# Kernel optimization log

Hardware: AMD Instinct MI355X
Metric: run time of the kernel (lower is better)

## Reference

```python
import jax, jax.numpy as jnp
import numpy as np

B, N, D = 4, 2048, 1024
H, HD = 16, 64          # heads, head dim
ROT = 64                # rotary dims (full head)
SCALE = HD ** -0.5


def _rotate_half(x):
    # interleaved pair rotation: (c r) with r=2 -> (-x2, x1)
    x = x.reshape(x.shape[:-1] + (-1, 2))
    x1, x2 = x[..., 0], x[..., 1]
    return jnp.stack((-x2, x1), axis=-1).reshape(x.shape[:-2] + (-1,))


def _rope(t, pos_enc):
    # t: [b,h,n,c], pos_enc: [1,n,rot] -> broadcast over heads
    pe = pos_enc[:, None, : t.shape[-2], :]          # [1,1,n,rot]
    t_rot, t_pass = t[..., :ROT], t[..., ROT:]
    t_rot = t_rot * jnp.cos(pe) + _rotate_half(t_rot) * jnp.sin(pe)
    return jnp.concatenate((t_rot, t_pass), axis=-1)


def setup_inputs() -> dict:
    key = jax.random.key(0)
    ks = jax.random.split(key, 16)
    s = 0.02
    return {
        "query": jax.random.normal(ks[0], (B, N, D), jnp.float32),
        "key": jax.random.normal(ks[1], (B, N, D), jnp.float32),
        "value": jax.random.normal(ks[2], (B, N, D), jnp.float32),
        "pad_mask": jax.random.randint(ks[3], (B, N), 0, 2) > 0,
        "pos_enc": jax.random.uniform(ks[4], (1, N, ROT), jnp.float32),
        "Wq": jax.random.normal(ks[5], (D, D), jnp.float32) * s,
        "bq": jnp.zeros((D,), jnp.float32),
        "Wk": jax.random.normal(ks[6], (D, D), jnp.float32) * s,
        "bk": jnp.zeros((D,), jnp.float32),
        "Wv": jax.random.normal(ks[7], (D, D), jnp.float32) * s,
        "bv": jnp.zeros((D,), jnp.float32),
        "Wo": jax.random.normal(ks[8], (D, D), jnp.float32) * s,
        "bo": jnp.zeros((D,), jnp.float32),
    }


def reference(query, key, value, pad_mask, pos_enc, Wq, bq, Wk, bk, Wv, bv, Wo, bo):
    def split_heads(x):
        return x.reshape(x.shape[0], x.shape[1], H, HD).transpose(0, 2, 1, 3)  # b h n c

    q = split_heads(query @ Wq + bq) * SCALE
    k = split_heads(key @ Wk + bk)
    v = split_heads(value @ Wv + bv)

    q = _rope(q, pos_enc)
    k = _rope(k, pos_enc)

    attn = jnp.einsum("bhic,bhjc->bhij", q, k)
    neg = -jnp.finfo(attn.dtype).max
    attn = jnp.where(pad_mask[:, None, None, :], neg, attn)
    attn = jax.nn.softmax(attn, axis=-1)

    o = jnp.einsum("bhij,bhjc->bhic", attn, v)
    o = o.transpose(0, 2, 1, 3).reshape(o.shape[0], o.shape[2], H * HD)  # b n (h c)
    return o @ Wo + bo
```

## Files before the change

kernel.cpp:

```cpp
#include <hip/hip_runtime.h>

#define B_ 4
#define N_ 2048
#define D_ 1024
#define H_ 16
#define HD_ 64
#define QSCALE_ 0.18033688011112042f

typedef __bf16 bf16x8 __attribute__((ext_vector_type(8)));
typedef float f32x4 __attribute__((ext_vector_type(4)));

#if __has_builtin(__builtin_amdgcn_exp2f)
#define EXP2(x) __builtin_amdgcn_exp2f(x)
#else
#define EXP2(x) exp2f(x)
#endif

__device__ __forceinline__ f32x4 mfma16(bf16x8 a, bf16x8 b, f32x4 c) {
    return __builtin_amdgcn_mfma_f32_16x16x32_bf16(a, b, c, 0, 0, 0);
}

__device__ __forceinline__ void gload16(const void* g, void* l) {
    __builtin_amdgcn_global_load_lds(
        (const __attribute__((address_space(1))) void*)g,
        (__attribute__((address_space(3))) void*)l, 16, 0, 0);
}

__device__ __forceinline__ unsigned pack2(float x, float y) {
    __bf16 a = (__bf16)x, b = (__bf16)y;
    unsigned ua = __builtin_bit_cast(unsigned short, a);
    unsigned ub = __builtin_bit_cast(unsigned short, b);
    return ua | (ub << 16);
}

__global__ void prep_kernel(const float* __restrict__ pe, const int* __restrict__ mask,
                            unsigned* __restrict__ cstab, float* __restrict__ maskf) {
    int i = blockIdx.x * 256 + threadIdx.x;
    if (i < N_ * HD_) {
        float v = pe[i];
        __bf16 cb = (__bf16)cosf(v), sb = (__bf16)sinf(v);
        unsigned cu = __builtin_bit_cast(unsigned short, cb);
        unsigned su = __builtin_bit_cast(unsigned short, sb);
        cstab[i] = cu | (su << 16);
    }
    if (i < B_ * N_) maskf[i] = mask[i] ? -1e30f : 0.0f;
}

__global__ __launch_bounds__(256) void tw_kernel(const float* __restrict__ W, __bf16* __restrict__ Wt) {
    __shared__ float T[64][65];
    const int k0 = blockIdx.x * 64, n0 = blockIdx.y * 64;
    const int t = threadIdx.x;
#pragma unroll
    for (int i = 0; i < 4; ++i) {
        int row = i * 16 + (t >> 4);
        int c4 = (t & 15) * 4;
        float4 v = *(const float4*)(W + (size_t)(k0 + row) * D_ + n0 + c4);
        T[row][c4] = v.x; T[row][c4 + 1] = v.y; T[row][c4 + 2] = v.z; T[row][c4 + 3] = v.w;
    }
    __syncthreads();
#pragma unroll
    for (int i = 0; i < 2; ++i) {
        int task = i * 256 + t;
        int nrow = task >> 3, ks = task & 7;
        bf16x8 o;
#pragma unroll
        for (int e = 0; e < 8; ++e) o[e] = (__bf16)T[ks * 8 + e][nrow];
        *(bf16x8*)(Wt + (size_t)(n0 + nrow) * D_ + k0 + ks * 8) = o;
    }
}

__global__ __launch_bounds__(256) void tw3_kernel(
    const float* __restrict__ W0, const float* __restrict__ W1, const float* __restrict__ W2,
    __bf16* __restrict__ T0, __bf16* __restrict__ T1, __bf16* __restrict__ T2)
{
    const float* W = (blockIdx.z == 0) ? W0 : (blockIdx.z == 1) ? W1 : W2;
    __bf16* Wt = (blockIdx.z == 0) ? T0 : (blockIdx.z == 1) ? T1 : T2;
    __shared__ float T[64][65];
    const int k0 = blockIdx.x * 64, n0 = blockIdx.y * 64;
    const int t = threadIdx.x;
#pragma unroll
    for (int i = 0; i < 4; ++i) {
        int row = i * 16 + (t >> 4);
        int c4 = (t & 15) * 4;
        float4 v = *(const float4*)(W + (size_t)(k0 + row) * D_ + n0 + c4);
        T[row][c4] = v.x; T[row][c4 + 1] = v.y; T[row][c4 + 2] = v.z; T[row][c4 + 3] = v.w;
    }
    __syncthreads();
#pragma unroll
    for (int i = 0; i < 2; ++i) {
        int task = i * 256 + t;
        int nrow = task >> 3, ks = task & 7;
        bf16x8 o;
#pragma unroll
        for (int e = 0; e < 8; ++e) o[e] = (__bf16)T[ks * 8 + e][nrow];
        *(bf16x8*)(Wt + (size_t)(n0 + nrow) * D_ + k0 + ks * 8) = o;
    }
}

__global__ __launch_bounds__(256) void proj_v5(
    const float* __restrict__ Xq, const float* __restrict__ Xk, const float* __restrict__ Xv,
    const __bf16* __restrict__ WtQ, const __bf16* __restrict__ WtK, const __bf16* __restrict__ WtV,
    const float* __restrict__ bQ, const float* __restrict__ bK, const float* __restrict__ bV,
    const unsigned* __restrict__ cstab,
    __bf16* __restrict__ dq, __bf16* __restrict__ dk, __bf16* __restrict__ dv)
{
    __shared__ __align__(16) char smem[35072];
    __bf16* As = (__bf16*)smem;
    __bf16* Bs = (__bf16*)(smem + 16384);

    const int which = blockIdx.y >> 3;
    const float* X    = (which == 0) ? Xq  : (which == 1) ? Xk  : Xv;
    const __bf16* Wt  = (which == 0) ? WtQ : (which == 1) ? WtK : WtV;
    const float* bias = (which == 0) ? bQ  : (which == 1) ? bK  : bV;
    __bf16* dst       = (which == 0) ? dq  : (which == 1) ? dk  : dv;
    const int mode = which;

    const int tid = threadIdx.x;
    const int lane = tid & 63, w = tid >> 6;
    const int wr = w >> 1, wc = w & 1;
    const int r16 = lane & 15, g = lane >> 4;
    const int m0 = blockIdx.x * 128;
    const int n0 = (blockIdx.y & 7) * 128;
    const int srow8 = tid >> 3, slot = tid & 7;

    f32x4 acc[4][4];
#pragma unroll
    for (int m = 0; m < 4; ++m)
#pragma unroll
        for (int n = 0; n < 4; ++n) acc[m][n] = (f32x4){0.f, 0.f, 0.f, 0.f};

    for (int kt = 0; kt < 16; ++kt) {
        float4 va0[4], va1[4];
#pragma unroll
        for (int i = 0; i < 4; ++i) {
            int row = i * 32 + srow8;
            const float* s = X + (size_t)(m0 + row) * D_ + kt * 64 + slot * 8;
            va0[i] = *(const float4*)s;
            va1[i] = *(const float4*)(s + 4);
        }
#pragma unroll
        for (int j = 0; j < 4; ++j) {
            int row = j * 32 + srow8;
            const char* src = (const char*)Wt + ((size_t)(n0 + row) * D_ + kt * 64) * 2
                              + ((slot ^ (row & 7)) << 4);
            gload16(src, (char*)Bs + j * 4096 + w * 1024);
        }
#pragma unroll
        for (int i = 0; i < 4; ++i) {
            int row = i * 32 + srow8;
            bf16x8 bv;
            bv[0] = (__bf16)va0[i].x; bv[1] = (__bf16)va0[i].y;
            bv[2] = (__bf16)va0[i].z; bv[3] = (__bf16)va0[i].w;
            bv[4] = (__bf16)va1[i].x; bv[5] = (__bf16)va1[i].y;
            bv[6] = (__bf16)va1[i].z; bv[7] = (__bf16)va1[i].w;
            *(bf16x8*)((char*)As + row * 128 + ((slot ^ (row & 7)) << 4)) = bv;
        }
        __syncthreads();
#pragma unroll
        for (int kk = 0; kk < 2; ++kk) {
            bf16x8 aF[4], bF[4];
#pragma unroll
            for (int m = 0; m < 4; ++m) {
                int row = wr * 64 + m * 16 + r16;
                aF[m] = *(const bf16x8*)((char*)As + row * 128 + (((kk * 4 + g) ^ (row & 7)) << 4));
            }
#pragma unroll
            for (int n = 0; n < 4; ++n) {
                int row = wc * 64 + n * 16 + r16;
                bF[n] = *(const bf16x8*)((char*)Bs + row * 128 + (((kk * 4 + g) ^ (row & 7)) << 4));
            }
#pragma unroll
            for (int m = 0; m < 4; ++m)
#pragma unroll
                for (int n = 0; n < 4; ++n)
                    acc[m][n] = mfma16(aF[m], bF[n], acc[m][n]);
        }
        __syncthreads();
    }

    if (mode <= 1) {
#pragma unroll
        for (int m = 0; m < 4; ++m)
#pragma unroll
            for (int n = 0; n < 4; ++n) {
                int col = n0 + wc * 64 + n * 16 + r16;
                int h = col >> 6, hd = col & 63;
#pragma unroll
                for (int j = 0; j < 4; ++j) {
                    int bn = m0 + wr * 64 + m * 16 + g * 4 + j;
                    int np = bn & (N_ - 1), b = bn >> 11;
                    float val = acc[m][n][j] + bias[col];
                    if (mode == 0) val *= QSCALE_;
                    float other = __shfl_xor(val, 1);
                    unsigned cs = cstab[np * HD_ + hd];
                    float c = __uint_as_float(cs << 16);
                    float sn = __uint_as_float(cs & 0xffff0000u);
                    val = val * c + ((col & 1) ? other : -other) * sn;
                    dst[((size_t)(b * H_ + h) * N_ + np) * HD_ + hd] = (__bf16)val;
                }
            }
    } else {
        __bf16* T = (__bf16*)smem;
#pragma unroll
        for (int m = 0; m < 4; ++m)
#pragma unroll
            for (int n = 0; n < 4; ++n) {
                int c = wc * 64 + n * 16 + r16;
                float bs = bias[n0 + c];
#pragma unroll
                for (int j = 0; j < 4; ++j) {
                    int sr = wr * 64 + m * 16 + g * 4 + j;
                    T[c * 136 + sr] = (__bf16)(acc[m][n][j] + bs);
                }
            }
        __syncthreads();
        const int b = m0 >> 11, np0 = m0 & (N_ - 1);
#pragma unroll
        for (int i = 0; i < 8; ++i) {
            int task = i * 256 + tid;
            int trow = task >> 4, ch = task & 15;
            int colg = n0 + trow;
            int h = colg >> 6, hd = colg & 63;
            bf16x8 vv = *(const bf16x8*)&T[trow * 136 + ch * 8];
            *(bf16x8*)(dst + (((size_t)(b * H_ + h) * HD_ + hd) * N_ + np0 + ch * 8)) = vv;
        }
    }
}

__global__ __launch_bounds__(256, 4) void attn_v6(
    const __bf16* __restrict__ qws, const __bf16* __restrict__ kws,
    const __bf16* __restrict__ vtws, const float* __restrict__ maskf,
    __bf16* __restrict__ ows)
{
    __shared__ __align__(16) __bf16 Ks0[4096], Ks1[4096];
    __shared__ __align__(16) __bf16 Vs0[4096], Vs1[4096];
    __shared__ __align__(16) char Pbuf[8192];

    const int tid = threadIdx.x;
    const int lane = tid & 63, w = tid >> 6;
    const int r16 = lane & 15, g = lane >> 4;

    const int lid = blockIdx.x;
    const int virt = (lid & 7) * 128 + (lid >> 3);
    const int bh = virt >> 4;
    const int b = bh >> 4, h = bh & 15;
    const int q0 = (virt & 15) * 128;
    const int srow8 = tid >> 3, slot = tid & 7;

    bf16x8 qF[2][2];
#pragma unroll
    for (int qq = 0; qq < 2; ++qq) {
        const __bf16* qb = qws + ((size_t)bh * N_ + q0 + w * 32 + qq * 16 + r16) * HD_ + g * 8;
        qF[qq][0] = *(const bf16x8*)qb;
        qF[qq][1] = *(const bf16x8*)(qb + 32);
    }

    bf16x8 onesF;
#pragma unroll
    for (int e = 0; e < 8; ++e) onesF[e] = (__bf16)1.0f;

    const char* kbase = (const char*)(kws + (size_t)bh * N_ * HD_);
    const char* vbase = (const char*)(vtws + (size_t)bh * HD_ * N_);
    const float* mbase = maskf + b * N_;
    char* Pw = Pbuf + w * 2048;

    f32x4 o[2][4];
    f32x4 lacc[2];
#pragma unroll
    for (int qq = 0; qq < 2; ++qq) {
        lacc[qq] = (f32x4){0.f, 0.f, 0.f, 0.f};
#pragma unroll
        for (int n = 0; n < 4; ++n) o[qq][n] = (f32x4){0.f, 0.f, 0.f, 0.f};
    }

#define STAGE_(KD, VD, kt) {                                                          \
    _Pragma("unroll")                                                                 \
    for (int j = 0; j < 2; ++j) {                                                     \
        int row = j * 32 + srow8;                                                     \
        gload16(kbase + (size_t)((kt) * 64 + row) * 128 + ((slot ^ (row & 7)) << 4),  \
                (char*)(KD) + j * 4096 + w * 1024);                                   \
    }                                                                                 \
    _Pragma("unroll")                                                                 \
    for (int j = 0; j < 2; ++j) {                                                     \
        int row = j * 32 + srow8;                                                     \
        gload16(vbase + (size_t)row * (N_ * 2) + (kt) * 128 + ((slot ^ (row & 7)) << 4), \
                (char*)(VD) + j * 4096 + w * 1024);                                   \
    } }

#define TILE_(KB, VB, KN, VN, kt) {                                                   \
    if ((kt) + 1 < 32) STAGE_(KN, VN, (kt) + 1);                                      \
    f32x4 s0[4], s1[4];                                                               \
    _Pragma("unroll")                                                                 \
    for (int n = 0; n < 4; ++n) {                                                     \
        f32x4 mb = *(const f32x4*)(mbase + (kt) * 64 + n * 16 + g * 4);               \
        s0[n] = mb; s1[n] = mb;                                                       \
    }                                                                                 \
    __builtin_amdgcn_s_setprio(1);                                                    \
    _Pragma("unroll")                                                                 \
    for (int n = 0; n < 4; ++n) {                                                     \
        int row = n * 16 + r16;                                                       \
        bf16x8 kF0 = *(const bf16x8*)((const char*)(KB) + row * 128 + ((g ^ (row & 7)) << 4));        \
        bf16x8 kF1 = *(const bf16x8*)((const char*)(KB) + row * 128 + (((4 + g) ^ (row & 7)) << 4));  \
        s0[n] = mfma16(kF0, qF[0][0], s0[n]);                                         \
        s0[n] = mfma16(kF1, qF[0][1], s0[n]);                                         \
        s1[n] = mfma16(kF0, qF[1][0], s1[n]);                                         \
        s1[n] = mfma16(kF1, qF[1][1], s1[n]);                                         \
    }                                                                                 \
    __builtin_amdgcn_s_setprio(0);                                                    \
    bf16x8 pF0[2], pF1[2];                                                            \
    _Pragma("unroll")                                                                 \
    for (int n = 0; n < 4; ++n) {                                                     \
        int u0 = ((n * 2 + (g >> 1)) ^ (r16 & 7));                                    \
        int off = (g & 1) * 2;                                                        \
        *(unsigned*)(Pw + r16 * 128 + u0 * 16 + off * 4)       = pack2(EXP2(s0[n][0]), EXP2(s0[n][1])); \
        *(unsigned*)(Pw + r16 * 128 + u0 * 16 + (off + 1) * 4) = pack2(EXP2(s0[n][2]), EXP2(s0[n][3])); \
    }                                                                                 \
    _Pragma("unroll")                                                                 \
    for (int kk = 0; kk < 2; ++kk)                                                    \
        pF0[kk] = *(const bf16x8*)(Pw + r16 * 128 + (((kk * 4 + g) ^ (r16 & 7)) << 4)); \
    lacc[0] = mfma16(onesF, pF0[0], lacc[0]);                                         \
    lacc[0] = mfma16(onesF, pF0[1], lacc[0]);                                         \
    _Pragma("unroll")                                                                 \
    for (int n = 0; n < 4; ++n) {                                                     \
        int u0 = ((n * 2 + (g >> 1)) ^ (r16 & 7));                                    \
        int off = (g & 1) * 2;                                                        \
        *(unsigned*)(Pw + r16 * 128 + u0 * 16 + off * 4)       = pack2(EXP2(s1[n][0]), EXP2(s1[n][1])); \
        *(unsigned*)(Pw + r16 * 128 + u0 * 16 + (off + 1) * 4) = pack2(EXP2(s1[n][2]), EXP2(s1[n][3])); \
    }                                                                                 \
    _Pragma("unroll")                                                                 \
    for (int kk = 0; kk < 2; ++kk)                                                    \
        pF1[kk] = *(const bf16x8*)(Pw + r16 * 128 + (((kk * 4 + g) ^ (r16 & 7)) << 4)); \
    lacc[1] = mfma16(onesF, pF1[0], lacc[1]);                                         \
    lacc[1] = mfma16(onesF, pF1[1], lacc[1]);                                         \
    __builtin_amdgcn_s_setprio(1);                                                    \
    _Pragma("unroll")                                                                 \
    for (int n = 0; n < 4; ++n) {                                                     \
        int row = n * 16 + r16;                                                       \
        bf16x8 vF0 = *(const bf16x8*)((const char*)(VB) + row * 128 + ((g ^ (row & 7)) << 4));        \
        bf16x8 vF1 = *(const bf16x8*)((const char*)(VB) + row * 128 + (((4 + g) ^ (row & 7)) << 4));  \
        o[0][n] = mfma16(vF0, pF0[0], o[0][n]);                                       \
        o[0][n] = mfma16(vF1, pF0[1], o[0][n]);                                       \
        o[1][n] = mfma16(vF0, pF1[0], o[1][n]);                                       \
        o[1][n] = mfma16(vF1, pF1[1], o[1][n]);                                       \
    }                                                                                 \
    __builtin_amdgcn_s_setprio(0);                                                    \
    __syncthreads(); }

    STAGE_(Ks0, Vs0, 0);
    __syncthreads();

    for (int kt = 0; kt < 32; kt += 2) {
        TILE_(Ks0, Vs0, Ks1, Vs1, kt);
        TILE_(Ks1, Vs1, Ks0, Vs0, kt + 1);
    }
#undef TILE_
#undef STAGE_

#pragma unroll
    for (int qq = 0; qq < 2; ++qq) {
        float inv = 1.0f / lacc[qq][0];
#pragma unroll
        for (int n = 0; n < 4; ++n) {
            int u0 = ((n * 2 + (g >> 1)) ^ (r16 & 7));
            int off = (g & 1) * 2;
            *(unsigned*)(Pw + r16 * 128 + u0 * 16 + off * 4)       = pack2(o[qq][n][0] * inv, o[qq][n][1] * inv);
            *(unsigned*)(Pw + r16 * 128 + u0 * 16 + (off + 1) * 4) = pack2(o[qq][n][2] * inv, o[qq][n][3] * inv);
        }
        int qrow = q0 + w * 32 + qq * 16 + r16;
#pragma unroll
        for (int kk = 0; kk < 2; ++kk) {
            bf16x8 v = *(const bf16x8*)(Pw + r16 * 128 + (((kk * 4 + g) ^ (r16 & 7)) << 4));
            *(bf16x8*)(ows + ((size_t)(b * N_ + qrow)) * D_ + h * HD_ + kk * 32 + g * 8) = v;
        }
    }
}

__global__ __launch_bounds__(256) void gemm_out_v2(
    const __bf16* __restrict__ A, const __bf16* __restrict__ Wt,
    const float* __restrict__ bias, float* __restrict__ out)
{
    __shared__ __align__(16) __bf16 As[8192], Bs[8192];

    const int tid = threadIdx.x;
    const int lane = tid & 63, w = tid >> 6;
    const int wr = w >> 1, wc = w & 1;
    const int r16 = lane & 15, g = lane >> 4;
    const int m0 = blockIdx.x * 128;
    const int n0 = blockIdx.y * 128;
    const int srow8 = tid >> 3, slot = tid & 7;

    f32x4 acc[4][4];
#pragma unroll
    for (int m = 0; m < 4; ++m)
#pragma unroll
        for (int n = 0; n < 4; ++n) acc[m][n] = (f32x4){0.f, 0.f, 0.f, 0.f};

    for (int kt = 0; kt < 16; ++kt) {
#pragma unroll
        for (int j = 0; j < 4; ++j) {
            int row = j * 32 + srow8;
            const char* srcA = (const char*)A + ((size_t)(m0 + row) * D_ + kt * 64) * 2
                               + ((slot ^ (row & 7)) << 4);
            gload16(srcA, (char*)As + j * 4096 + w * 1024);
            const char* srcB = (const char*)Wt + ((size_t)(n0 + row) * D_ + kt * 64) * 2
                               + ((slot ^ (row & 7)) << 4);
            gload16(srcB, (char*)Bs + j * 4096 + w * 1024);
        }
        __syncthreads();
#pragma unroll
        for (int kk = 0; kk < 2; ++kk) {
            bf16x8 aF[4], bF[4];
#pragma unroll
            for (int m = 0; m < 4; ++m) {
                int row = wr * 64 + m * 16 + r16;
                aF[m] = *(const bf16x8*)((char*)As + row * 128 + (((kk * 4 + g) ^ (row & 7)) << 4));
            }
#pragma unroll
            for (int n = 0; n < 4; ++n) {
                int row = wc * 64 + n * 16 + r16;
                bF[n] = *(const bf16x8*)((char*)Bs + row * 128 + (((kk * 4 + g) ^ (row & 7)) << 4));
            }
#pragma unroll
            for (int m = 0; m < 4; ++m)
#pragma unroll
                for (int n = 0; n < 4; ++n)
                    acc[m][n] = mfma16(aF[m], bF[n], acc[m][n]);
        }
        __syncthreads();
    }

#pragma unroll
    for (int m = 0; m < 4; ++m)
#pragma unroll
        for (int n = 0; n < 4; ++n) {
            int col = n0 + wc * 64 + n * 16 + r16;
            float bs = bias[col];
#pragma unroll
            for (int j = 0; j < 4; ++j) {
                int bn = m0 + wr * 64 + m * 16 + g * 4 + j;
                out[(size_t)bn * D_ + col] = acc[m][n][j] + bs;
            }
        }
}

extern "C" void kernel_launch(void* const* d_in, const int* in_sizes, int n_in,
                              void* d_out, int out_size, void* d_ws, size_t ws_size,
                              hipStream_t stream)
{
    const float* query = (const float*)d_in[0];
    const float* key   = (const float*)d_in[1];
    const float* value = (const float*)d_in[2];
    const int* mask    = (const int*)d_in[3];
    const float* pos_enc = (const float*)d_in[4];
    const float* Wq = (const float*)d_in[5];
    const float* bq = (const float*)d_in[6];
    const float* Wk = (const float*)d_in[7];
    const float* bk = (const float*)d_in[8];
    const float* Wv = (const float*)d_in[9];
    const float* bv = (const float*)d_in[10];
    const float* Wo = (const float*)d_in[11];
    const float* bo = (const float*)d_in[12];
    float* out = (float*)d_out;

    char* ws = (char*)d_ws;
    const size_t MB16 = (size_t)16 * 1024 * 1024;
    const size_t need = 4 * MB16 + 524288 + 32768;
    if (ws_size < need) return;

    __bf16* qws   = (__bf16*)(ws);
    __bf16* kws   = (__bf16*)(ws + MB16);
    __bf16* vtws  = (__bf16*)(ws + 2 * MB16);
    __bf16* ows   = (__bf16*)(ws + 3 * MB16);
    unsigned* cstab = (unsigned*)(ws + 4 * MB16);
    float* maskf  = (float*)(ws + 4 * MB16 + 524288);
    __bf16* wtQ   = (__bf16*)(ws + 3 * MB16);
    __bf16* wtK   = wtQ + (size_t)D_ * D_;
    __bf16* wtV   = wtK + (size_t)D_ * D_;
    __bf16* wtO   = (__bf16*)(ws);

    hipLaunchKernelGGL(prep_kernel, dim3(512), dim3(256), 0, stream, pos_enc, mask, cstab, maskf);

    dim3 gt3(16, 16, 3);
    dim3 gt(16, 16);
    hipLaunchKernelGGL(tw3_kernel, gt3, dim3(256), 0, stream, Wq, Wk, Wv, wtQ, wtK, wtV);

    hipLaunchKernelGGL(proj_v5, dim3(64, 24), dim3(256), 0, stream,
                       query, key, value, wtQ, wtK, wtV, bq, bk, bv, cstab, qws, kws, vtws);

    hipLaunchKernelGGL(attn_v6, dim3(1024), dim3(256), 0, stream,
                       qws, kws, vtws, maskf, ows);

    hipLaunchKernelGGL(tw_kernel, gt, dim3(256), 0, stream, Wo, wtO);
    hipLaunchKernelGGL(gemm_out_v2, dim3(64, 8), dim3(256), 0, stream, ows, wtO, bo, out);
}
```

Measured before the change: 217.0 us.

## Pre-cast QKV inputs to bf16 and load A tiles via direct global-to-LDS

Adds a kernel that converts query, key and value from fp32 to bf16 once, so the projection GEMM can fetch its A operand with asynchronous global_load_lds into swizzled LDS. This replaces the per-tile register load and convert step. All four weight transposes are merged into one launch. The cost is an extra full pass over the activations, a larger workspace, and a fallback to the old path when the workspace is too small.

```diff
diff --git a/kernel.cpp b/kernel.cpp
--- a/kernel.cpp
+++ b/kernel.cpp
@@ -46,6 +46,21 @@
     if (i < B_ * N_) maskf[i] = mask[i] ? -1e30f : 0.0f;
 }
 
+__global__ __launch_bounds__(256) void cast3_kernel(
+    const float* __restrict__ q, const float* __restrict__ k, const float* __restrict__ v,
+    __bf16* __restrict__ xb)
+{
+    const float* src = (blockIdx.y == 0) ? q : (blockIdx.y == 1) ? k : v;
+    __bf16* dst = xb + (size_t)blockIdx.y * 8388608;
+    size_t i = ((size_t)blockIdx.x * 256 + threadIdx.x) * 8;
+    float4 a = *(const float4*)(src + i);
+    float4 b = *(const float4*)(src + i + 4);
+    bf16x8 o;
+    o[0] = (__bf16)a.x; o[1] = (__bf16)a.y; o[2] = (__bf16)a.z; o[3] = (__bf16)a.w;
+    o[4] = (__bf16)b.x; o[5] = (__bf16)b.y; o[6] = (__bf16)b.z; o[7] = (__bf16)b.w;
+    *(bf16x8*)(dst + i) = o;
+}
+
 __global__ __launch_bounds__(256) void tw_kernel(const float* __restrict__ W, __bf16* __restrict__ Wt) {
     __shared__ float T[64][65];
     const int k0 = blockIdx.x * 64, n0 = blockIdx.y * 64;
@@ -97,8 +112,38 @@
     }
 }
 
-__global__ __launch_bounds__(256) void proj_v5(
-    const float* __restrict__ Xq, const float* __restrict__ Xk, const float* __restrict__ Xv,
+__global__ __launch_bounds__(256) void tw4_kernel(
+    const float* __restrict__ W0, const float* __restrict__ W1,
+    const float* __restrict__ W2, const float* __restrict__ W3,
+    __bf16* __restrict__ T0, __bf16* __restrict__ T1,
+    __bf16* __restrict__ T2, __bf16* __restrict__ T3)
+{
+    const float* W = (blockIdx.z == 0) ? W0 : (blockIdx.z == 1) ? W1 : (blockIdx.z == 2) ? W2 : W3;
+    __bf16* Wt = (blockIdx.z == 0) ? T0 : (blockIdx.z == 1) ? T1 : (blockIdx.z == 2) ? T2 : T3;
+    __shared__ float T[64][65];
+    const int k0 = blockIdx.x * 64, n0 = blockIdx.y * 64;
+    const int t = threadIdx.x;
+#pragma unroll
+    for (int i = 0; i < 4; ++i) {
+        int row = i * 16 + (t >> 4);
+        int c4 = (t & 15) * 4;
+        float4 v = *(const float4*)(W + (size_t)(k0 + row) * D_ + n0 + c4);
+        T[row][c4] = v.x; T[row][c4 + 1] = v.y; T[row][c4 + 2] = v.z; T[row][c4 + 3] = v.w;
+    }
+    __syncthreads();
+#pragma unroll
+    for (int i = 0; i < 2; ++i) {
+        int task = i * 256 + t;
+        int nrow = task >> 3, ks = task & 7;
+        bf16x8 o;
+#pragma unroll
+        for (int e = 0; e < 8; ++e) o[e] = (__bf16)T[ks * 8 + e][nrow];
+        *(bf16x8*)(Wt + (size_t)(n0 + nrow) * D_ + k0 + ks * 8) = o;
+    }
+}
+
+__global__ __launch_bounds__(256) void proj_v6(
+    const __bf16* __restrict__ Xb,
     const __bf16* __restrict__ WtQ, const __bf16* __restrict__ WtK, const __bf16* __restrict__ WtV,
     const float* __restrict__ bQ, const float* __restrict__ bK, const float* __restrict__ bV,
     const unsigned* __restrict__ cstab,
@@ -109,7 +154,7 @@
     __bf16* Bs = (__bf16*)(smem + 16384);
 
     const int which = blockIdx.y >> 3;
-    const float* X    = (which == 0) ? Xq  : (which == 1) ? Xk  : Xv;
+    const __bf16* X   = Xb + (size_t)which * 8388608;
     const __bf16* Wt  = (which == 0) ? WtQ : (which == 1) ? WtK : WtV;
     const float* bias = (which == 0) ? bQ  : (which == 1) ? bK  : bV;
     __bf16* dst       = (which == 0) ? dq  : (which == 1) ? dk  : dv;
@@ -130,30 +175,15 @@
         for (int n = 0; n < 4; ++n) acc[m][n] = (f32x4){0.f, 0.f, 0.f, 0.f};
 
     for (int kt = 0; kt < 16; ++kt) {
-        float4 va0[4], va1[4];
-#pragma unroll
-        for (int i = 0; i < 4; ++i) {
-            int row = i * 32 + srow8;
-            const float* s = X + (size_t)(m0 + row) * D_ + kt * 64 + slot * 8;
-            va0[i] = *(const float4*)s;
-            va1[i] = *(const float4*)(s + 4);
-        }
 #pragma unroll
         for (int j = 0; j < 4; ++j) {
             int row = j * 32 + srow8;
-            const char* src = (const char*)Wt + ((size_t)(n0 + row) * D_ + kt * 64) * 2
-                              + ((slot ^ (row & 7)) << 4);
-            gload16(src, (char*)Bs + j * 4096 + w * 1024);
-        }
-#pragma unroll
-        for (int i = 0; i < 4; ++i) {
-            int row = i * 32 + srow8;
-            bf16x8 bv;
-            bv[0] = (__bf16)va0[i].x; bv[1] = (__bf16)va0[i].y;
-            bv[2] = (__bf16)va0[i].z; bv[3] = (__bf16)va0[i].w;
-            bv[4] = (__bf16)va1[i].x; bv[5] = (__bf16)va1[i].y;
-            bv[6] = (__bf16)va1[i].z; bv[7] = (__bf16)va1[i].w;
-            *(bf16x8*)((char*)As + row * 128 + ((slot ^ (row & 7)) << 4)) = bv;
+            const char* srcA = (const char*)X + ((size_t)(m0 + row) * D_ + kt * 64) * 2
+                               + ((slot ^ (row & 7)) << 4);
+            gload16(srcA, (char*)As + j * 4096 + w * 1024);
+            const char* srcB = (const char*)Wt + ((size_t)(n0 + row) * D_ + kt * 64) * 2
+                               + ((slot ^ (row & 7)) << 4);
+            gload16(srcB, (char*)Bs + j * 4096 + w * 1024);
         }
         __syncthreads();
 #pragma unroll
@@ -201,6 +231,138 @@
             }
     } else {
         __bf16* T = (__bf16*)smem;
+        __syncthreads();
+#pragma unroll
+        for (int m = 0; m < 4; ++m)
+#pragma unroll
+            for (int n = 0; n < 4; ++n) {
+                int c = wc * 64 + n * 16 + r16;
+                float bs = bias[n0 + c];
+#pragma unroll
+                for (int j = 0; j < 4; ++j) {
+                    int sr = wr * 64 + m * 16 + g * 4 + j;
+                    T[c * 136 + sr] = (__bf16)(acc[m][n][j] + bs);
+                }
+            }
+        __syncthreads();
+        const int b = m0 >> 11, np0 = m0 & (N_ - 1);
+#pragma unroll
+        for (int i = 0; i < 8; ++i) {
+            int task = i * 256 + tid;
+            int trow = task >> 4, ch = task & 15;
+            int colg = n0 + trow;
+            int h = colg >> 6, hd = colg & 63;
+            bf16x8 vv = *(const bf16x8*)&T[trow * 136 + ch * 8];
+            *(bf16x8*)(dst + (((size_t)(b * H_ + h) * HD_ + hd) * N_ + np0 + ch * 8)) = vv;
+        }
+    }
+}
+
+__global__ __launch_bounds__(256) void proj_v5(
+    const float* __restrict__ Xq, const float* __restrict__ Xk, const float* __restrict__ Xv,
+    const __bf16* __restrict__ WtQ, const __bf16* __restrict__ WtK, const __bf16* __restrict__ WtV,
+    const float* __restrict__ bQ, const float* __restrict__ bK, const float* __restrict__ bV,
+    const unsigned* __restrict__ cstab,
+    __bf16* __restrict__ dq, __bf16* __restrict__ dk, __bf16* __restrict__ dv)
+{
+    __shared__ __align__(16) char smem[35072];
+    __bf16* As = (__bf16*)smem;
+    __bf16* Bs = (__bf16*)(smem + 16384);
+
+    const int which = blockIdx.y >> 3;
+    const float* X    = (which == 0) ? Xq  : (which == 1) ? Xk  : Xv;
+    const __bf16* Wt  = (which == 0) ? WtQ : (which == 1) ? WtK : WtV;
+    const float* bias = (which == 0) ? bQ  : (which == 1) ? bK  : bV;
+    __bf16* dst       = (which == 0) ? dq  : (which == 1) ? dk  : dv;
+    const int mode = which;
+
+    const int tid = threadIdx.x;
+    const int lane = tid & 63, w = tid >> 6;
+    const int wr = w >> 1, wc = w & 1;
+    const int r16 = lane & 15, g = lane >> 4;
+    const int m0 = blockIdx.x * 128;
+    const int n0 = (blockIdx.y & 7) * 128;
+    const int srow8 = tid >> 3, slot = tid & 7;
+
+    f32x4 acc[4][4];
+#pragma unroll
+    for (int m = 0; m < 4; ++m)
+#pragma unroll
+        for (int n = 0; n < 4; ++n) acc[m][n] = (f32x4){0.f, 0.f, 0.f, 0.f};
+
+    for (int kt = 0; kt < 16; ++kt) {
+        float4 va0[4], va1[4];
+#pragma unroll
+        for (int i = 0; i < 4; ++i) {
+            int row = i * 32 + srow8;
+            const float* s = X + (size_t)(m0 + row) * D_ + kt * 64 + slot * 8;
+            va0[i] = *(const float4*)s;
+            va1[i] = *(const float4*)(s + 4);
+        }
+#pragma unroll
+        for (int j = 0; j < 4; ++j) {
+            int row = j * 32 + srow8;
+            const char* src = (const char*)Wt + ((size_t)(n0 + row) * D_ + kt * 64) * 2
+                              + ((slot ^ (row & 7)) << 4);
+            gload16(src, (char*)Bs + j * 4096 + w * 1024);
+        }
+#pragma unroll
+        for (int i = 0; i < 4; ++i) {
+            int row = i * 32 + srow8;
+            bf16x8 bv;
+            bv[0] = (__bf16)va0[i].x; bv[1] = (__bf16)va0[i].y;
+            bv[2] = (__bf16)va0[i].z; bv[3] = (__bf16)va0[i].w;
+            bv[4] = (__bf16)va1[i].x; bv[5] = (__bf16)va1[i].y;
+            bv[6] = (__bf16)va1[i].z; bv[7] = (__bf16)va1[i].w;
+            *(bf16x8*)((char*)As + row * 128 + ((slot ^ (row & 7)) << 4)) = bv;
+        }
+        __syncthreads();
+#pragma unroll
+        for (int kk = 0; kk < 2; ++kk) {
+            bf16x8 aF[4], bF[4];
+#pragma unroll
+            for (int m = 0; m < 4; ++m) {
+                int row = wr * 64 + m * 16 + r16;
+                aF[m] = *(const bf16x8*)((char*)As + row * 128 + (((kk * 4 + g) ^ (row & 7)) << 4));
+            }
+#pragma unroll
+            for (int n = 0; n < 4; ++n) {
+                int row = wc * 64 + n * 16 + r16;
+                bF[n] = *(const bf16x8*)((char*)Bs + row * 128 + (((kk * 4 + g) ^ (row & 7)) << 4));
+            }
+#pragma unroll
+            for (int m = 0; m < 4; ++m)
+#pragma unroll
+                for (int n = 0; n < 4; ++n)
+                    acc[m][n] = mfma16(aF[m], bF[n], acc[m][n]);
+        }
+        __syncthreads();
+    }
+
+    if (mode <= 1) {
+#pragma unroll
+        for (int m = 0; m < 4; ++m)
+#pragma unroll
+            for (int n = 0; n < 4; ++n) {
+                int col = n0 + wc * 64 + n * 16 + r16;
+                int h = col >> 6, hd = col & 63;
+#pragma unroll
+                for (int j = 0; j < 4; ++j) {
+                    int bn = m0 + wr * 64 + m * 16 + g * 4 + j;
+                    int np = bn & (N_ - 1), b = bn >> 11;
+                    float val = acc[m][n][j] + bias[col];
+                    if (mode == 0) val *= QSCALE_;
+                    float other = __shfl_xor(val, 1);
+                    unsigned cs = cstab[np * HD_ + hd];
+                    float c = __uint_as_float(cs << 16);
+                    float sn = __uint_as_float(cs & 0xffff0000u);
+                    val = val * c + ((col & 1) ? other : -other) * sn;
+                    dst[((size_t)(b * H_ + h) * N_ + np) * HD_ + hd] = (__bf16)val;
+                }
+            }
+    } else {
+        __bf16* T = (__bf16*)smem;
+        __syncthreads();
 #pragma unroll
         for (int m = 0; m < 4; ++m)
 #pragma unroll
@@ -464,32 +626,52 @@
 
     char* ws = (char*)d_ws;
     const size_t MB16 = (size_t)16 * 1024 * 1024;
-    const size_t need = 4 * MB16 + 524288 + 32768;
-    if (ws_size < need) return;
-
-    __bf16* qws   = (__bf16*)(ws);
-    __bf16* kws   = (__bf16*)(ws + MB16);
-    __bf16* vtws  = (__bf16*)(ws + 2 * MB16);
-    __bf16* ows   = (__bf16*)(ws + 3 * MB16);
-    unsigned* cstab = (unsigned*)(ws + 4 * MB16);
-    float* maskf  = (float*)(ws + 4 * MB16 + 524288);
-    __bf16* wtQ   = (__bf16*)(ws + 3 * MB16);
-    __bf16* wtK   = wtQ + (size_t)D_ * D_;
-    __bf16* wtV   = wtK + (size_t)D_ * D_;
-    __bf16* wtO   = (__bf16*)(ws);
-
-    hipLaunchKernelGGL(prep_kernel, dim3(512), dim3(256), 0, stream, pos_enc, mask, cstab, maskf);
-
-    dim3 gt3(16, 16, 3);
-    dim3 gt(16, 16);
-    hipLaunchKernelGGL(tw3_kernel, gt3, dim3(256), 0, stream, Wq, Wk, Wv, wtQ, wtK, wtV);
-
-    hipLaunchKernelGGL(proj_v5, dim3(64, 24), dim3(256), 0, stream,
-                       query, key, value, wtQ, wtK, wtV, bq, bk, bv, cstab, qws, kws, vtws);
-
-    hipLaunchKernelGGL(attn_v6, dim3(1024), dim3(256), 0, stream,
-                       qws, kws, vtws, maskf, ows);
-
-    hipLaunchKernelGGL(tw_kernel, gt, dim3(256), 0, stream, Wo, wtO);
-    hipLaunchKernelGGL(gemm_out_v2, dim3(64, 8), dim3(256), 0, stream, ows, wtO, bo, out);
-}
+    const size_t MB2  = (size_t)2 * 1024 * 1024;
+    const size_t need_big = 3 * MB16 + 4 * MB16 + 4 * MB2 + 524288 + 32768;
+    const size_t need_small = 4 * MB16 + 524288 + 32768;
+
+    if (ws_size >= need_big) {
+        __bf16* Xb    = (__bf16*)(ws);
+        __bf16* qws   = (__bf16*)(ws + 3 * MB16);
+        __bf16* kws   = (__bf16*)(ws + 4 * MB16);
+        __bf16* vtws  = (__bf16*)(ws + 5 * MB16);
+        __bf16* ows   = (__bf16*)(ws + 6 * MB16);
+        __bf16* wtQ   = (__bf16*)(ws + 7 * MB16);
+        __bf16* wtK   = (__bf16*)(ws + 7 * MB16 + MB2);
+        __bf16* wtV   = (__bf16*)(ws + 7 * MB16 + 2 * MB2);
+        __bf16* wtO   = (__bf16*)(ws + 7 * MB16 + 3 * MB2);
+        unsigned* cstab = (unsigned*)(ws + 7 * MB16 + 4 * MB2);
+        float* maskf  = (float*)(ws + 7 * MB16 + 4 * MB2 + 524288);
+
+        hipLaunchKernelGGL(prep_kernel, dim3(512), dim3(256), 0, stream, pos_enc, mask, cstab, maskf);
+        hipLaunchKernelGGL(cast3_kernel, dim3(4096, 3), dim3(256), 0, stream, query, key, value, Xb);
+        hipLaunchKernelGGL(tw4_kernel, dim3(16, 16, 4), dim3(256), 0, stream,
+                           Wq, Wk, Wv, Wo, wtQ, wtK, wtV, wtO);
+        hipLaunchKernelGGL(proj_v6, dim3(64, 24), dim3(256), 0, stream,
+                           Xb, wtQ, wtK, wtV, bq, bk, bv, cstab, qws, kws, vtws);
+        hipLaunchKernelGGL(attn_v6, dim3(1024), dim3(256), 0, stream,
+                           qws, kws, vtws, maskf, ows);
+        hipLaunchKernelGGL(gemm_out_v2, dim3(64, 8), dim3(256), 0, stream, ows, wtO, bo, out);
+    } else {
+        if (ws_size < need_small) return;
+        __bf16* qws   = (__bf16*)(ws);
+        __bf16* kws   = (__bf16*)(ws + MB16);
+        __bf16* vtws  = (__bf16*)(ws + 2 * MB16);
+        __bf16* ows   = (__bf16*)(ws + 3 * MB16);
+        unsigned* cstab = (unsigned*)(ws + 4 * MB16);
+        float* maskf  = (float*)(ws + 4 * MB16 + 524288);
+        __bf16* wtQ   = (__bf16*)(ws + 3 * MB16);
+        __bf16* wtK   = wtQ + (size_t)D_ * D_;
+        __bf16* wtV   = wtK + (size_t)D_ * D_;
+        __bf16* wtO   = (__bf16*)(ws);
+
+        hipLaunchKernelGGL(prep_kernel, dim3(512), dim3(256), 0, stream, pos_enc, mask, cstab, maskf);
+        hipLaunchKernelGGL(tw3_kernel, dim3(16, 16, 3), dim3(256), 0, stream, Wq, Wk, Wv, wtQ, wtK, wtV);
+        hipLaunchKernelGGL(proj_v5, dim3(64, 24), dim3(256), 0, stream,
+                           query, key, value, wtQ, wtK, wtV, bq, bk, bv, cstab, qws, kws, vtws);
+        hipLaunchKernelGGL(attn_v6, dim3(1024), dim3(256), 0, stream,
+                           qws, kws, vtws, maskf, ows);
+        hipLaunchKernelGGL(tw_kernel, dim3(16, 16), dim3(256), 0, stream, Wo, wtO);
+        hipLaunchKernelGGL(gemm_out_v2, dim3(64, 8), dim3(256), 0, stream, ows, wtO, bo, out);
+    }
+}
```

After: 220.1 us. About the same (+1.4%).
